# Kernel tuning notes

Hardware: AMD Instinct MI355X
Metric: run time of the kernel (lower is better)

## Reference

```python
import jax, jax.numpy as jnp
import numpy as np

E = 100000    # number of edges
T = 1000000   # number of triplets
D = 128       # embed_dim
NB = 20       # n_basis (angle expansion width)
EPS = 1e-6


def setup_inputs() -> dict:
    key = jax.random.key(0)
    ks = jax.random.split(key, 14)
    def lin(k, fan_in, fan_out):
        # torch.nn.Linear default init: U(-1/sqrt(fan_in), 1/sqrt(fan_in))
        bound = 1.0 / np.sqrt(fan_in)
        kw, kb = jax.random.split(k)
        W = jax.random.uniform(kw, (fan_in, fan_out), jnp.float32, -bound, bound)
        b = jax.random.uniform(kb, (fan_out,), jnp.float32, -bound, bound)
        return W, b
    edge_attr = jax.random.normal(ks[0], (E, D), jnp.float32)
    edge_vectors = jax.random.normal(ks[1], (E, 3), jnp.float32)
    three_body_indices = jax.random.randint(ks[2], (T, 3), 0, 50000, jnp.int64)
    three_body_edge_indices = jax.random.randint(ks[3], (T, 2), 0, E, jnp.int64)
    Wa1, ba1 = lin(ks[4], 3, NB)          # SimpleMLPAngleExpansion layer 1
    Wa2, ba2 = lin(ks[5], NB, NB)         # SimpleMLPAngleExpansion layer 2
    W1, b1 = lin(ks[6], 2 * D + NB, D)    # phi_3b layer 1
    W2, b2 = lin(ks[7], D, D)             # phi_3b layer 2
    Wu, bu = lin(ks[8], D, D)             # update_edge
    return {
        "edge_attr": edge_attr,
        "three_body_indices": three_body_indices,
        "three_body_edge_indices": three_body_edge_indices,
        "edge_vectors": edge_vectors,
        "Wa1": Wa1, "ba1": ba1, "Wa2": Wa2, "ba2": ba2,
        "W1": W1, "b1": b1, "W2": W2, "b2": b2,
        "Wu": Wu, "bu": bu,
    }


def reference(edge_attr, three_body_indices, three_body_edge_indices, edge_vectors,
              Wa1, ba1, Wa2, ba2, W1, b1, W2, b2, Wu, bu):
    e_ij = three_body_edge_indices[:, 0]
    e_ik = three_body_edge_indices[:, 1]
    # gather edge vectors for the two edges forming the angle (sign-flipped)
    vec_ij = -edge_vectors[e_ij]           # (T, 3)
    vec_ik = -edge_vectors[e_ik]           # (T, 3)
    len_ij = jnp.maximum(jnp.linalg.norm(vec_ij, axis=1, keepdims=True), EPS)
    len_ik = jnp.maximum(jnp.linalg.norm(vec_ik, axis=1, keepdims=True), EPS)
    cos_t = jnp.clip(jnp.sum(vec_ij * vec_ik, axis=1, keepdims=True) / (len_ij * len_ik), -1.0, 1.0)
    # SimpleMLPAngleExpansion: (T,3) -> (T, NB)
    ang_in = jnp.concatenate([len_ij, len_ik, cos_t], axis=-1)
    angle_feats = jax.nn.silu(ang_in @ Wa1 + ba1) @ Wa2 + ba2
    # triplet features: gathered edge embeddings + angle features
    h_3b = jnp.concatenate([edge_attr[e_ij], edge_attr[e_ik], angle_feats], axis=-1)  # (T, 2D+NB)
    h_3b = jnp.nan_to_num(h_3b, nan=0.0, posinf=0.0, neginf=0.0)
    # phi_3b: Linear -> SiLU -> Linear
    m_ijk = jax.nn.silu(h_3b @ W1 + b1) @ W2 + b2   # (T, D)
    # scatter-add messages back to edge ij
    delta = jax.ops.segment_sum(m_ijk, e_ij, num_segments=edge_attr.shape[0])  # (E, D)
    return jnp.nan_to_num(delta @ Wu + bu, nan=0.0, posinf=0.0, neginf=0.0)
```

## Files before the change

### kernel.cpp

```cpp
#include <hip/hip_runtime.h>
#include <stdint.h>

#define NB 20
#define EG 16

typedef __attribute__((ext_vector_type(8))) short bf16x8;
typedef __attribute__((ext_vector_type(4))) float f32x4;

__device__ __forceinline__ float bf_lo(uint32_t u) { return __uint_as_float(u << 16); }
__device__ __forceinline__ float bf_hi(uint32_t u) { return __uint_as_float(u & 0xffff0000u); }
__device__ __forceinline__ uint32_t f2bf(float f) {
    uint32_t u = __float_as_uint(f);
    return (u + 0x7fffu + ((u >> 16) & 1u)) >> 16;
}
__device__ __forceinline__ uint32_t pack_bf2(float a, float b) {
    return f2bf(a) | (f2bf(b) << 16);
}
__device__ __forceinline__ float silu_f(float x) {
    float e = __builtin_amdgcn_exp2f(-1.4426950408889634f * x);
    return x * __builtin_amdgcn_rcpf(1.f + e);
}

__global__ void prep_kernel(const float* __restrict__ W2, const float* __restrict__ b2,
                            const float* __restrict__ Wu,
                            float* __restrict__ Mf32, float* __restrict__ cvec) {
    int q = threadIdx.x;
    int k = blockIdx.x;
    const float* row = (k < 128) ? (W2 + k * 128) : b2;
    float acc0 = 0.f, acc1 = 0.f;
    for (int j = 0; j < 128; ++j) {
        float w = row[j];
        float2 wu = *(const float2*)(Wu + j * 128 + 2 * q);
        acc0 = fmaf(w, wu.x, acc0);
        acc1 = fmaf(w, wu.y, acc1);
    }
    if (k < 128) {
        Mf32[k * 128 + 2 * q] = acc0;
        Mf32[k * 128 + 2 * q + 1] = acc1;
    } else {
        cvec[2 * q] = acc0;
        cvec[2 * q + 1] = acc1;
    }
}

__global__ void prep2(const float* __restrict__ W1, uint32_t* __restrict__ Bpk) {
    int d = blockIdx.x * 256 + threadIdx.x;
    int q = d & 3, l = (d >> 2) & 63, c = (d >> 8) & 15, s = d >> 12;
    int k = 32 * s + ((l >> 4) << 3) + (q << 1);
    int col = (c << 4) + (l & 15);
    int r0 = (col < 128) ? k : (k + 128);
    int cc = col & 127;
    float v0 = W1[(size_t)r0 * 128 + cc];
    float v1 = W1[(size_t)(r0 + 1) * 128 + cc];
    Bpk[d] = pack_bf2(v0, v1);
}

__global__ void prepM(const float* __restrict__ Mf32, uint32_t* __restrict__ Mfrag) {
    int d = blockIdx.x * 256 + threadIdx.x;
    int q = d & 3, l = (d >> 2) & 63, c = (d >> 8) & 7, s = d >> 11;
    int k = 32 * s + ((l >> 4) << 3) + (q << 1);
    int col = (c << 4) + (l & 15);
    Mfrag[d] = pack_bf2(Mf32[k * 128 + col], Mf32[(k + 1) * 128 + col]);
}

__global__ void __launch_bounds__(256) kA3(const float* __restrict__ edge_attr,
                                           const uint32_t* __restrict__ Bpk,
                                           uint16_t* __restrict__ Pb, int E) {
    __shared__ uint32_t As[4096];
    __shared__ uint32_t Bs[16384];
    const int tid = threadIdx.x;
    const int e0 = blockIdx.x * 64;
    const int nE = min(64, E - e0);

    for (int d = tid; d < 4096; d += 256) {
        int row = d >> 6, p = d & 63;
        int g = p >> 2;
        float2 v;
        if (row < nE) v = *(const float2*)(edge_attr + (size_t)(e0 + row) * 128 + 2 * p);
        else { v.x = 0.f; v.y = 0.f; }
        As[row * 64 + ((g ^ (row & 7)) << 2) + (p & 3)] = pack_bf2(v.x, v.y);
    }
    for (int d = tid; d < 4096; d += 256)
        ((uint4*)Bs)[d] = ((const uint4*)Bpk)[d];
    __syncthreads();

    const int w = tid >> 6, l = tid & 63;

    bf16x8 afr[4][4];
#pragma unroll
    for (int rb = 0; rb < 4; ++rb)
#pragma unroll
        for (int s = 0; s < 4; ++s) {
            int row = rb * 16 + (l & 15);
            int g = s * 4 + (l >> 4);
            afr[rb][s] = *(const bf16x8*)((const char*)As + row * 256 + ((g ^ (row & 7)) << 4));
        }

    f32x4 acc[4][4];
#pragma unroll
    for (int cl = 0; cl < 4; ++cl)
#pragma unroll
        for (int rb = 0; rb < 4; ++rb) acc[cl][rb] = (f32x4)(0.f);

#pragma unroll
    for (int cl = 0; cl < 4; ++cl) {
        const int c = w * 4 + cl;
#pragma unroll
        for (int s = 0; s < 4; ++s) {
            bf16x8 bfr = *(const bf16x8*)((const char*)Bs + (((s * 16 + c) * 64 + l) << 4));
#pragma unroll
            for (int rb = 0; rb < 4; ++rb)
                acc[cl][rb] = __builtin_amdgcn_mfma_f32_16x16x32_bf16(afr[rb][s], bfr, acc[cl][rb], 0, 0, 0);
        }
    }

#pragma unroll
    for (int cl = 0; cl < 4; ++cl)
#pragma unroll
        for (int rb = 0; rb < 4; ++rb)
#pragma unroll
            for (int r = 0; r < 4; ++r) {
                int row = rb * 16 + (l >> 4) * 4 + r;
                if (row < nE)
                    Pb[(size_t)(e0 + row) * 256 + w * 64 + cl * 16 + (l & 15)] = (uint16_t)f2bf(acc[cl][rb][r]);
            }
}

__global__ void khist(const int* __restrict__ tbe, uint32_t* __restrict__ cnt, int T) {
    int t = blockIdx.x * blockDim.x + threadIdx.x;
    int stride = gridDim.x * blockDim.x;
    for (; t < T; t += stride) {
        int2 ee = ((const int2*)tbe)[t];
        atomicAdd(&cnt[ee.x], 1u);
    }
}

__global__ void scanA(const uint32_t* __restrict__ cnt, uint32_t* __restrict__ bsum, int E) {
    __shared__ uint32_t s[256];
    int tid = threadIdx.x;
    int e = blockIdx.x * 256 + tid;
    s[tid] = (e < E) ? cnt[e] : 0u;
    __syncthreads();
    for (int off = 128; off > 0; off >>= 1) {
        if (tid < off) s[tid] += s[tid + off];
        __syncthreads();
    }
    if (tid == 0) bsum[blockIdx.x] = s[0];
}

__global__ void scanB(uint32_t* __restrict__ bsum, int n) {
    __shared__ uint32_t s[512];
    int tid = threadIdx.x;
    s[tid] = (tid < n) ? bsum[tid] : 0u;
    __syncthreads();
    for (int off = 1; off < 512; off <<= 1) {
        uint32_t a = (tid >= off) ? s[tid - off] : 0u;
        __syncthreads();
        s[tid] += a;
        __syncthreads();
    }
    if (tid < n) bsum[tid] = (tid > 0) ? s[tid - 1] : 0u;
}

__global__ void scanC(const uint32_t* __restrict__ cnt, const uint32_t* __restrict__ bsum,
                      uint32_t* __restrict__ offs, int E) {
    __shared__ uint32_t s[256];
    int tid = threadIdx.x;
    int e = blockIdx.x * 256 + tid;
    uint32_t v = (e < E) ? cnt[e] : 0u;
    s[tid] = v;
    __syncthreads();
    for (int off = 1; off < 256; off <<= 1) {
        uint32_t a = (tid >= off) ? s[tid - off] : 0u;
        __syncthreads();
        s[tid] += a;
        __syncthreads();
    }
    if (e < E) offs[e] = bsum[blockIdx.x] + s[tid] - v;
}

__global__ void __launch_bounds__(256) kSA(const int* __restrict__ tbe,
                                           const float* __restrict__ evec,
                                           const float* __restrict__ Wa1,
                                           const float* __restrict__ ba1,
                                           const float* __restrict__ Wa2,
                                           const float* __restrict__ ba2,
                                           uint32_t* __restrict__ offs,
                                           uint32_t* __restrict__ afpk,
                                           uint32_t* __restrict__ sortedT, int T) {
    __shared__ float wa1_s[60], ba1_s[NB], wa2_s[400], ba2_s[NB];
    const int tid = threadIdx.x;
    for (int i = tid; i < 400; i += 256) wa2_s[i] = Wa2[i];
    if (tid < 60) wa1_s[tid] = Wa1[tid];
    if (tid < NB) { ba1_s[tid] = ba1[tid]; ba2_s[tid] = ba2[tid]; }
    __syncthreads();

    const int t = blockIdx.x * 256 + tid;
    if (t >= T) return;

    int2 ee = ((const int2*)tbe)[t];
    const float ax = evec[ee.x * 3], ay = evec[ee.x * 3 + 1], az = evec[ee.x * 3 + 2];
    const float bx = evec[ee.y * 3], by = evec[ee.y * 3 + 1], bz = evec[ee.y * 3 + 2];
    const float li = fmaxf(__builtin_amdgcn_sqrtf(ax * ax + ay * ay + az * az), 1e-6f);
    const float lk = fmaxf(__builtin_amdgcn_sqrtf(bx * bx + by * by + bz * bz), 1e-6f);
    float ct = (ax * bx + ay * by + az * bz) * __builtin_amdgcn_rcpf(li * lk);
    ct = fminf(fmaxf(ct, -1.f), 1.f);

    float h[NB];
#pragma unroll
    for (int o = 0; o < NB; ++o) {
        float z = fmaf(li, wa1_s[o], fmaf(lk, wa1_s[20 + o], fmaf(ct, wa1_s[40 + o], ba1_s[o])));
        h[o] = silu_f(z);
    }
    float af[NB];
#pragma unroll
    for (int o2 = 0; o2 < NB; ++o2) af[o2] = ba2_s[o2];
#pragma unroll
    for (int o = 0; o < NB; ++o) {
#pragma unroll
        for (int o2 = 0; o2 < NB; ++o2) af[o2] = fmaf(h[o], wa2_s[o * 20 + o2], af[o2]);
    }

    const uint32_t pos = atomicAdd(&offs[ee.x], 1u);
    sortedT[pos] = (uint32_t)t;
    uint32_t* dst = afpk + (size_t)t * 10;
#pragma unroll
    for (int j = 0; j < 5; ++j) {
        uint2 pk;
        pk.x = pack_bf2(af[4 * j], af[4 * j + 1]);
        pk.y = pack_bf2(af[4 * j + 2], af[4 * j + 3]);
        *(uint2*)(dst + 2 * j) = pk;
    }
}

__global__ void __launch_bounds__(256) kB6(const uint32_t* __restrict__ sortedT,
                                           const uint32_t* __restrict__ offs,
                                           const int* __restrict__ tbe,
                                           const float* __restrict__ W1,
                                           const float* __restrict__ b1,
                                           const uint32_t* __restrict__ Ppk,
                                           const uint32_t* __restrict__ afpk,
                                           float* __restrict__ S, int E) {
    __shared__ __align__(16) float af_s[4][64 * 20];
    __shared__ uint32_t e2_s[4][64];

    const int tid = threadIdx.x;
    const int wave = tid >> 6, lane = tid & 63;
    const int gw = blockIdx.x * 4 + wave;
    const int eb = gw * EG;
    if (eb >= E) return;
    const int ee = min(eb + EG, E);

    uint32_t offv = 0u;
    {
        int oi = eb - 1 + lane;
        if (lane <= EG && oi >= 0) offv = offs[min(oi, E - 1)];
    }
    const uint32_t tstart = __shfl(offv, 0);
    const uint32_t tend = __shfl(offv, ee - eb);

    float2 wreg[NB];
#pragma unroll
    for (int k = 0; k < NB; ++k)
        wreg[k] = *(const float2*)(W1 + (size_t)(256 + k) * 128 + 2 * lane);
    const float2 b1v = ((const float2*)b1)[lane];

    int ecur = eb;
    uint32_t eend = __shfl(offv, 1);
    uint32_t p1A = Ppk[(size_t)ecur * 128 + lane];
    uint32_t p1B = Ppk[(size_t)min(ecur + 1, E - 1) * 128 + lane];
    float p1lo = bf_lo(p1A) + b1v.x;
    float p1hi = bf_hi(p1A) + b1v.y;
    float acc0 = 0.f, acc1 = 0.f;

    float* afw = af_s[wave];

    for (uint32_t base = tstart; base < tend; base += 64u) {
        const int m = min(64, (int)(tend - base));
        const uint32_t idx = min(base + (uint32_t)lane, tend - 1u);
        const uint32_t st = sortedT[idx];
        e2_s[wave][lane] = (uint32_t)(((const int2*)tbe)[st].y);
#pragma unroll
        for (int k = 0; k < 10; ++k) {
            int i = lane + 64 * k;
            int r = i / 10;
            int c = i - r * 10;
            uint32_t str = __shfl(st, r);
            uint32_t u = afpk[(size_t)str * 10 + c];
            afw[2 * i] = bf_lo(u);
            afw[2 * i + 1] = bf_hi(u);
        }
        asm volatile("s_waitcnt lgkmcnt(0)" ::: "memory");
        __builtin_amdgcn_sched_barrier(0);

        uint32_t p2a = Ppk[(size_t)e2_s[wave][0] * 128 + 64 + lane];
        uint32_t p2b = (m > 1) ? Ppk[(size_t)e2_s[wave][1] * 128 + 64 + lane] : p2a;
        int i2 = 0;
        while (i2 < m) {
            const uint32_t rem = eend - base;
            const int lim = (rem < (uint32_t)m) ? (int)rem : m;
            for (; i2 < lim; ++i2) {
                const uint32_t p2 = p2a;
                p2a = p2b;
                if (i2 + 2 < m) p2b = Ppk[(size_t)e2_s[wave][i2 + 2] * 128 + 64 + lane];
                float x0 = p1lo + bf_lo(p2);
                float x1 = p1hi + bf_hi(p2);
                const float4* afp = (const float4*)(afw + i2 * 20);
                const float4 fA = afp[0], fB = afp[1], fC = afp[2], fD = afp[3], fE = afp[4];
                const float a_[20] = {fA.x, fA.y, fA.z, fA.w, fB.x, fB.y, fB.z, fB.w,
                                      fC.x, fC.y, fC.z, fC.w, fD.x, fD.y, fD.z, fD.w,
                                      fE.x, fE.y, fE.z, fE.w};
#pragma unroll
                for (int j = 0; j < NB; ++j) {
                    x0 = fmaf(a_[j], wreg[j].x, x0);
                    x1 = fmaf(a_[j], wreg[j].y, x1);
                }
                acc0 += silu_f(x0);
                acc1 += silu_f(x1);
            }
            if (base + (uint32_t)i2 == eend) {
                do {
                    float2 o;
                    o.x = acc0;
                    o.y = acc1;
                    ((float2*)S)[(size_t)ecur * 64 + lane] = o;
                    acc0 = 0.f;
                    acc1 = 0.f;
                    ++ecur;
                    if (ecur >= ee) { eend = 0xffffffffu; break; }
                    p1A = p1B;
                    p1B = Ppk[(size_t)min(ecur + 1, E - 1) * 128 + lane];
                    p1lo = bf_lo(p1A) + b1v.x;
                    p1hi = bf_hi(p1A) + b1v.y;
                    eend = __shfl(offv, ecur - eb + 1);
                } while (base + (uint32_t)i2 == eend);
            }
        }
    }
    while (ecur < ee) {
        float2 o;
        o.x = acc0;
        o.y = acc1;
        ((float2*)S)[(size_t)ecur * 64 + lane] = o;
        acc0 = 0.f;
        acc1 = 0.f;
        ++ecur;
    }
}

__global__ void __launch_bounds__(256) kC2(const float* __restrict__ S,
                                           const uint32_t* __restrict__ Mfrag,
                                           const float* __restrict__ cvec,
                                           const float* __restrict__ bu,
                                           const uint32_t* __restrict__ cnt,
                                           int E) {
    __shared__ uint32_t As[4096];
    __shared__ uint32_t Bs[8192];
    __shared__ float cnt_s[64];
    const int tid = threadIdx.x;
    const int e0 = blockIdx.x * 64;
    const int nE = min(64, E - e0);

    for (int d = tid; d < 4096; d += 256) {
        int row = d >> 6, p = d & 63;
        int g = p >> 2;
        float2 v;
        if (row < nE) v = *(const float2*)(S + (size_t)(e0 + row) * 128 + 2 * p);
        else { v.x = 0.f; v.y = 0.f; }
        As[row * 64 + ((g ^ (row & 7)) << 2) + (p & 3)] = pack_bf2(v.x, v.y);
    }
    for (int d = tid; d < 2048; d += 256)
        ((uint4*)Bs)[d] = ((const uint4*)Mfrag)[d];
    if (tid < 64) cnt_s[tid] = (tid < nE) ? (float)cnt[e0 + tid] : 0.f;
    __syncthreads();

    const int w = tid >> 6, l = tid & 63;

    bf16x8 afr[4][4];
#pragma unroll
    for (int rb = 0; rb < 4; ++rb)
#pragma unroll
        for (int s = 0; s < 4; ++s) {
            int row = rb * 16 + (l & 15);
            int g = s * 4 + (l >> 4);
            afr[rb][s] = *(const bf16x8*)((const char*)As + row * 256 + ((g ^ (row & 7)) << 4));
        }

    f32x4 acc[2][4];
#pragma unroll
    for (int cl = 0; cl < 2; ++cl)
#pragma unroll
        for (int rb = 0; rb < 4; ++rb) acc[cl][rb] = (f32x4)(0.f);

#pragma unroll
    for (int cl = 0; cl < 2; ++cl) {
        const int c = w * 2 + cl;
#pragma unroll
        for (int s = 0; s < 4; ++s) {
            bf16x8 bfr = *(const bf16x8*)((const char*)Bs + (((s * 8 + c) * 64 + l) << 4));
#pragma unroll
            for (int rb = 0; rb < 4; ++rb)
                acc[cl][rb] = __builtin_amdgcn_mfma_f32_16x16x32_bf16(afr[rb][s], bfr, acc[cl][rb], 0, 0, 0);
        }
    }

#pragma unroll
    for (int cl = 0; cl < 2; ++cl) {
        const int col = w * 32 + cl * 16 + (l & 15);
        const float cv = cvec[col];
        const float bv = bu[col];
#pragma unroll
        for (int rb = 0; rb < 4; ++rb)
#pragma unroll
            for (int r = 0; r < 4; ++r) {
                int row = rb * 16 + (l >> 4) * 4 + r;
                if (row < nE) {
                    float* dst = (float*)S + (size_t)(e0 + row) * 128 + col;
                    *dst = acc[cl][rb][r] + fmaf(cnt_s[row], cv, bv);
                }
            }
    }
}

extern "C" void kernel_launch(void* const* d_in, const int* in_sizes, int n_in,
                              void* d_out, int out_size, void* d_ws, size_t ws_size,
                              hipStream_t stream) {
    const float* edge_attr = (const float*)d_in[0];
    const int* tbe = (const int*)d_in[2];
    const float* evec = (const float*)d_in[3];
    const float* Wa1 = (const float*)d_in[4];
    const float* ba1 = (const float*)d_in[5];
    const float* Wa2 = (const float*)d_in[6];
    const float* ba2 = (const float*)d_in[7];
    const float* W1 = (const float*)d_in[8];
    const float* b1 = (const float*)d_in[9];
    const float* W2 = (const float*)d_in[10];
    const float* b2 = (const float*)d_in[11];
    const float* Wu = (const float*)d_in[12];
    const float* bu = (const float*)d_in[13];

    const int E = in_sizes[0] / 128;
    const int T = in_sizes[2] / 2;
    float* S = (float*)d_out;

    const int nScanBlk = (E + 255) / 256;

    char* ws = (char*)d_ws;
    size_t off = 0;
    uint32_t* Ppk = (uint32_t*)(ws + off); off += (size_t)E * 512;
    uint32_t* cnt = (uint32_t*)(ws + off); off += (size_t)E * 4;
    uint32_t* offs = (uint32_t*)(ws + off); off += (size_t)E * 4;
    uint32_t* sortedT = (uint32_t*)(ws + off); off += (size_t)T * 4;
    uint32_t* afpk = (uint32_t*)(ws + off); off += (size_t)T * 40;
    uint32_t* bsum = (uint32_t*)(ws + off); off += (size_t)((nScanBlk + 3) & ~3) * 4;
    uint32_t* Bpk = (uint32_t*)(ws + off); off += 65536;
    float* Mf32 = (float*)(ws + off); off += 65536;
    uint32_t* Mfrag = (uint32_t*)(ws + off); off += 32768;
    float* cvec = (float*)(ws + off); off += 512;

    hipMemsetAsync(cnt, 0, (size_t)E * 4, stream);

    prep_kernel<<<129, 64, 0, stream>>>(W2, b2, Wu, Mf32, cvec);
    prep2<<<64, 256, 0, stream>>>(W1, Bpk);
    prepM<<<32, 256, 0, stream>>>(Mf32, Mfrag);
    kA3<<<(E + 63) / 64, 256, 0, stream>>>(edge_attr, Bpk, (uint16_t*)Ppk, E);
    khist<<<2048, 256, 0, stream>>>(tbe, cnt, T);
    scanA<<<nScanBlk, 256, 0, stream>>>(cnt, bsum, E);
    scanB<<<1, 512, 0, stream>>>(bsum, nScanBlk);
    scanC<<<nScanBlk, 256, 0, stream>>>(cnt, bsum, offs, E);
    kSA<<<(T + 255) / 256, 256, 0, stream>>>(tbe, evec, Wa1, ba1, Wa2, ba2,
                                             offs, afpk, sortedT, T);
    const int nWaves = (E + EG - 1) / EG;
    kB6<<<(nWaves + 3) / 4, 256, 0, stream>>>(sortedT, offs, tbe, W1, b1, Ppk, afpk, S, E);
    kC2<<<(E + 63) / 64, 256, 0, stream>>>(S, Mfrag, cvec, bu, cnt, E);
}
```

Measured before the change: 562.9 us.

## Scatter angle features and partner edge into sorted order; fuse prep kernels

The angle-feature pass now writes its packed angle features and the second-edge index directly at the sorted (per-ij-edge) position. The main triplet kernel can then read them contiguously instead of doing an indirect sortedT gather followed by a tbe lookup. The two weight-prep kernels are merged into one launch, the histogram kernel reads two triplets per int4 load with half the blocks, and edges per wave drop from 16 to 8. This trades scattered writes in kSA for coalesced reads in the hot kernel. The histogram change assumes T is even.

```diff
diff --git a/kernel.cpp b/kernel.cpp
--- a/kernel.cpp
+++ b/kernel.cpp
@@ -2,7 +2,7 @@
 #include <stdint.h>
 
 #define NB 20
-#define EG 16
+#define EG 8
 
 typedef __attribute__((ext_vector_type(8))) short bf16x8;
 typedef __attribute__((ext_vector_type(4))) float f32x4;
@@ -21,38 +21,35 @@
     return x * __builtin_amdgcn_rcpf(1.f + e);
 }
 
-__global__ void prep_kernel(const float* __restrict__ W2, const float* __restrict__ b2,
-                            const float* __restrict__ Wu,
-                            float* __restrict__ Mf32, float* __restrict__ cvec) {
-    int q = threadIdx.x;
-    int k = blockIdx.x;
-    const float* row = (k < 128) ? (W2 + k * 128) : b2;
-    float acc0 = 0.f, acc1 = 0.f;
-    for (int j = 0; j < 128; ++j) {
-        float w = row[j];
-        float2 wu = *(const float2*)(Wu + j * 128 + 2 * q);
-        acc0 = fmaf(w, wu.x, acc0);
-        acc1 = fmaf(w, wu.y, acc1);
-    }
-    if (k < 128) {
-        Mf32[k * 128 + 2 * q] = acc0;
-        Mf32[k * 128 + 2 * q + 1] = acc1;
+__global__ void __launch_bounds__(256) prepA(const float* __restrict__ W2,
+                                             const float* __restrict__ b2,
+                                             const float* __restrict__ Wu,
+                                             const float* __restrict__ W1,
+                                             float* __restrict__ Mf32,
+                                             float* __restrict__ cvec,
+                                             uint32_t* __restrict__ Bpk) {
+    const int bid = blockIdx.x, tid = threadIdx.x;
+    if (bid < 65) {
+        int k = bid * 2 + (tid >> 7);
+        int col = tid & 127;
+        if (k <= 128) {
+            const float* row = (k < 128) ? (W2 + k * 128) : b2;
+            float acc = 0.f;
+            for (int j = 0; j < 128; ++j) acc = fmaf(row[j], Wu[j * 128 + col], acc);
+            if (k < 128) Mf32[k * 128 + col] = acc;
+            else cvec[col] = acc;
+        }
     } else {
-        cvec[2 * q] = acc0;
-        cvec[2 * q + 1] = acc1;
-    }
-}
-
-__global__ void prep2(const float* __restrict__ W1, uint32_t* __restrict__ Bpk) {
-    int d = blockIdx.x * 256 + threadIdx.x;
-    int q = d & 3, l = (d >> 2) & 63, c = (d >> 8) & 15, s = d >> 12;
-    int k = 32 * s + ((l >> 4) << 3) + (q << 1);
-    int col = (c << 4) + (l & 15);
-    int r0 = (col < 128) ? k : (k + 128);
-    int cc = col & 127;
-    float v0 = W1[(size_t)r0 * 128 + cc];
-    float v1 = W1[(size_t)(r0 + 1) * 128 + cc];
-    Bpk[d] = pack_bf2(v0, v1);
+        int d = (bid - 65) * 256 + tid;
+        int q = d & 3, l = (d >> 2) & 63, c = (d >> 8) & 15, s = d >> 12;
+        int k = 32 * s + ((l >> 4) << 3) + (q << 1);
+        int col = (c << 4) + (l & 15);
+        int r0 = (col < 128) ? k : (k + 128);
+        int cc = col & 127;
+        float v0 = W1[(size_t)r0 * 128 + cc];
+        float v1 = W1[(size_t)(r0 + 1) * 128 + cc];
+        Bpk[d] = pack_bf2(v0, v1);
+    }
 }
 
 __global__ void prepM(const float* __restrict__ Mf32, uint32_t* __restrict__ Mfrag) {
@@ -129,9 +126,11 @@
 __global__ void khist(const int* __restrict__ tbe, uint32_t* __restrict__ cnt, int T) {
     int t = blockIdx.x * blockDim.x + threadIdx.x;
     int stride = gridDim.x * blockDim.x;
-    for (; t < T; t += stride) {
-        int2 ee = ((const int2*)tbe)[t];
+    int half = T >> 1;
+    for (; t < half; t += stride) {
+        int4 ee = ((const int4*)tbe)[t];
         atomicAdd(&cnt[ee.x], 1u);
+        atomicAdd(&cnt[ee.z], 1u);
     }
 }
 
@@ -187,7 +186,7 @@
                                            const float* __restrict__ ba2,
                                            uint32_t* __restrict__ offs,
                                            uint32_t* __restrict__ afpk,
-                                           uint32_t* __restrict__ sortedT, int T) {
+                                           uint32_t* __restrict__ sortedE2, int T) {
     __shared__ float wa1_s[60], ba1_s[NB], wa2_s[400], ba2_s[NB];
     const int tid = threadIdx.x;
     for (int i = tid; i < 400; i += 256) wa2_s[i] = Wa2[i];
@@ -222,8 +221,8 @@
     }
 
     const uint32_t pos = atomicAdd(&offs[ee.x], 1u);
-    sortedT[pos] = (uint32_t)t;
-    uint32_t* dst = afpk + (size_t)t * 10;
+    sortedE2[pos] = (uint32_t)ee.y;
+    uint32_t* dst = afpk + (size_t)pos * 10;
 #pragma unroll
     for (int j = 0; j < 5; ++j) {
         uint2 pk;
@@ -233,9 +232,8 @@
     }
 }
 
-__global__ void __launch_bounds__(256) kB6(const uint32_t* __restrict__ sortedT,
+__global__ void __launch_bounds__(256) kB7(const uint32_t* __restrict__ sortedE2,
                                            const uint32_t* __restrict__ offs,
-                                           const int* __restrict__ tbe,
                                            const float* __restrict__ W1,
                                            const float* __restrict__ b1,
                                            const uint32_t* __restrict__ Ppk,
@@ -278,15 +276,10 @@
     for (uint32_t base = tstart; base < tend; base += 64u) {
         const int m = min(64, (int)(tend - base));
         const uint32_t idx = min(base + (uint32_t)lane, tend - 1u);
-        const uint32_t st = sortedT[idx];
-        e2_s[wave][lane] = (uint32_t)(((const int2*)tbe)[st].y);
-#pragma unroll
-        for (int k = 0; k < 10; ++k) {
-            int i = lane + 64 * k;
-            int r = i / 10;
-            int c = i - r * 10;
-            uint32_t str = __shfl(st, r);
-            uint32_t u = afpk[(size_t)str * 10 + c];
+        e2_s[wave][lane] = sortedE2[idx];
+        const uint32_t base10 = base * 10u;
+        for (int i = lane; i < m * 10; i += 64) {
+            const uint32_t u = afpk[base10 + i];
             afw[2 * i] = bf_lo(u);
             afw[2 * i + 1] = bf_hi(u);
         }
@@ -450,7 +443,7 @@
     uint32_t* Ppk = (uint32_t*)(ws + off); off += (size_t)E * 512;
     uint32_t* cnt = (uint32_t*)(ws + off); off += (size_t)E * 4;
     uint32_t* offs = (uint32_t*)(ws + off); off += (size_t)E * 4;
-    uint32_t* sortedT = (uint32_t*)(ws + off); off += (size_t)T * 4;
+    uint32_t* sortedE2 = (uint32_t*)(ws + off); off += (size_t)T * 4;
     uint32_t* afpk = (uint32_t*)(ws + off); off += (size_t)T * 40;
     uint32_t* bsum = (uint32_t*)(ws + off); off += (size_t)((nScanBlk + 3) & ~3) * 4;
     uint32_t* Bpk = (uint32_t*)(ws + off); off += 65536;
@@ -460,17 +453,16 @@
 
     hipMemsetAsync(cnt, 0, (size_t)E * 4, stream);
 
-    prep_kernel<<<129, 64, 0, stream>>>(W2, b2, Wu, Mf32, cvec);
-    prep2<<<64, 256, 0, stream>>>(W1, Bpk);
+    prepA<<<129, 256, 0, stream>>>(W2, b2, Wu, W1, Mf32, cvec, Bpk);
     prepM<<<32, 256, 0, stream>>>(Mf32, Mfrag);
     kA3<<<(E + 63) / 64, 256, 0, stream>>>(edge_attr, Bpk, (uint16_t*)Ppk, E);
-    khist<<<2048, 256, 0, stream>>>(tbe, cnt, T);
+    khist<<<1024, 256, 0, stream>>>(tbe, cnt, T);
     scanA<<<nScanBlk, 256, 0, stream>>>(cnt, bsum, E);
     scanB<<<1, 512, 0, stream>>>(bsum, nScanBlk);
     scanC<<<nScanBlk, 256, 0, stream>>>(cnt, bsum, offs, E);
     kSA<<<(T + 255) / 256, 256, 0, stream>>>(tbe, evec, Wa1, ba1, Wa2, ba2,
-                                             offs, afpk, sortedT, T);
+                                             offs, afpk, sortedE2, T);
     const int nWaves = (E + EG - 1) / EG;
-    kB6<<<(nWaves + 3) / 4, 256, 0, stream>>>(sortedT, offs, tbe, W1, b1, Ppk, afpk, S, E);
+    kB7<<<(nWaves + 3) / 4, 256, 0, stream>>>(sortedE2, offs, W1, b1, Ppk, afpk, S, E);
     kC2<<<(E + 63) / 64, 256, 0, stream>>>(S, Mfrag, cvec, bu, cnt, E);
 }
```

After: 497.9 us. 11.5% less time.
